# Kernel tuning notes

Measured on AMD Instinct MI355X. Metric: run time of the kernel, lower is better.

The kernel has to match this reference:

```python
import jax, jax.numpy as jnp
import numpy as np

B, H, S = 32, 128, 8192

def setup_inputs() -> dict:
    key = jax.random.key(0)
    k1, k2, k3, k4, k5 = jax.random.split(key, 5)
    return {
        "static_hidden": jax.random.normal(k1, (B, H, S), dtype=jnp.float32),
        "dynamic_hidden": jax.random.normal(k2, (B, H, S), dtype=jnp.float32),
        "decoder_hidden": jax.random.normal(k3, (B, H), dtype=jnp.float32),
        "v": jax.random.normal(k4, (1, 1, H), dtype=jnp.float32) * 0.01,
        "W": jax.random.normal(k5, (1, H, 3 * H), dtype=jnp.float32) * 0.01,
    }

def reference(static_hidden, dynamic_hidden, decoder_hidden, v, W):
    b, h, s = static_hidden.shape
    # concat (static, dynamic, expanded decoder) along feature dim -> [b, 3h, s]
    hidden = jnp.concatenate(
        [static_hidden, dynamic_hidden,
         jnp.broadcast_to(decoder_hidden[:, :, None], (b, h, s))], axis=1)
    # W[0]: [h, 3h]; tanh(W @ hidden) -> [b, h, s]
    e = jnp.tanh(jnp.einsum('hk,bks->bhs', W[0], hidden))
    # v[0,0]: [h]; scores -> [b, 1, s]
    scores = jnp.einsum('h,bhs->bs', v[0, 0], e)[:, None, :]
    return jax.nn.softmax(scores, axis=2)
```

## Files before the change

kernel.cpp:

```cpp
#include <hip/hip_runtime.h>
#include <math.h>

#define BB 32
#define HH 128
#define SS 8192

typedef __attribute__((ext_vector_type(8))) short bf8;
typedef __attribute__((ext_vector_type(4))) float f4;

static __device__ __forceinline__ unsigned short f2bf(float x) {
  union { float f; unsigned int u; } c; c.f = x;
  unsigned int r = c.u + 0x7FFFu + ((c.u >> 16) & 1u);
  return (unsigned short)(r >> 16);
}

__global__ __launch_bounds__(256) void prep_kernel(
    const float* __restrict__ W, const float* __restrict__ dec,
    unsigned short* __restrict__ Abf, float* __restrict__ bias) {
  const int b = blockIdx.x;
  const int tid = threadIdx.x;
  if (tid < HH) {
    const float* wr = W + (size_t)tid * 384 + 256;
    const float* db = dec + (size_t)b * HH;
    float acc = 0.f;
    #pragma unroll 8
    for (int j = 0; j < HH; ++j) acc += wr[j] * db[j];
    bias[b * HH + tid] = acc;
  }
  if (b == 0) {
    for (int idx = tid; idx < HH * 256; idx += 256) {
      int h = idx >> 8, k = idx & 255;
      Abf[idx] = f2bf(W[h * 384 + k]);
    }
  }
}

__global__ __launch_bounds__(256, 4) void attn_main(
    const float* __restrict__ sta, const float* __restrict__ dyn,
    const unsigned short* __restrict__ Abf, const float* __restrict__ bias,
    const float* __restrict__ v, float* __restrict__ scores) {
  const int tid  = threadIdx.x;
  const int l    = tid & 63;
  const int gw   = (blockIdx.x << 2) + (tid >> 6);
  const int b    = gw >> 8;
  const int tile = gw & 255;
  const int quad = l >> 4;
  const int n16  = l & 15;
  const int s0   = tile << 5;

  const size_t base = ((size_t)b << 20) + (size_t)(quad << 3) * SS + s0 + (n16 << 1);
  const float* p0 = sta + base;
  const float* p1 = dyn + base;

  f4 acc[8][2];
  #pragma unroll
  for (int mt = 0; mt < 8; ++mt) {
    acc[mt][0] = (f4){0.f, 0.f, 0.f, 0.f};
    acc[mt][1] = (f4){0.f, 0.f, 0.f, 0.f};
  }

  float2 bcur[8], bnxt[8];

  auto loadB = [&](int step, float2 (&dst)[8]) {
    const float* tp = (step < 4 ? p0 : p1) + ((size_t)((step & 3) << 5)) * SS;
    #pragma unroll
    for (int j = 0; j < 8; ++j)
      dst[j] = *(const float2*)(tp + (size_t)j * SS);
  };

  loadB(0, bcur);
  #pragma unroll
  for (int step = 0; step < 8; ++step) {
    if (step < 7) loadB(step + 1, bnxt);
    bf8 bfr0, bfr1;
    #pragma unroll
    for (int j = 0; j < 8; ++j) {
      bfr0[j] = (short)f2bf(bcur[j].x);
      bfr1[j] = (short)f2bf(bcur[j].y);
    }
    const unsigned short* abase = Abf + ((size_t)n16 << 8) + (step << 5) + (quad << 3);
    #pragma unroll
    for (int mt = 0; mt < 8; ++mt) {
      bf8 af = *(const bf8*)(abase + (mt << 12));
      acc[mt][0] = __builtin_amdgcn_mfma_f32_16x16x32_bf16(af, bfr0, acc[mt][0], 0, 0, 0);
      acc[mt][1] = __builtin_amdgcn_mfma_f32_16x16x32_bf16(af, bfr1, acc[mt][1], 0, 0, 0);
    }
    if (step < 7) {
      #pragma unroll
      for (int j = 0; j < 8; ++j) bcur[j] = bnxt[j];
    }
  }

  float part[2] = {0.f, 0.f};
  #pragma unroll
  for (int mt = 0; mt < 8; ++mt) {
    #pragma unroll
    for (int r = 0; r < 4; ++r) {
      const int h = mt * 16 + quad * 4 + r;
      const float bv = bias[(b << 7) + h];
      const float vv = v[h];
      part[0] += vv * tanhf(acc[mt][0][r] + bv);
      part[1] += vv * tanhf(acc[mt][1][r] + bv);
    }
  }
  part[0] += __shfl_xor(part[0], 16, 64);
  part[0] += __shfl_xor(part[0], 32, 64);
  part[1] += __shfl_xor(part[1], 16, 64);
  part[1] += __shfl_xor(part[1], 32, 64);
  if (quad == 0) {
    float2 o = make_float2(part[0], part[1]);
    *(float2*)(scores + ((size_t)b << 13) + s0 + (n16 << 1)) = o;
  }
}

__global__ __launch_bounds__(1024) void softmax_kernel(float* __restrict__ out) {
  const int b = blockIdx.x;
  const int tid = threadIdx.x;
  float* row = out + ((size_t)b << 13);
  float4 x0 = ((const float4*)row)[tid];
  float4 x1 = ((const float4*)row)[tid + 1024];
  float lmax = fmaxf(fmaxf(fmaxf(x0.x, x0.y), fmaxf(x0.z, x0.w)),
                     fmaxf(fmaxf(x1.x, x1.y), fmaxf(x1.z, x1.w)));
  __shared__ float red[17];
  #pragma unroll
  for (int o = 32; o >= 1; o >>= 1) lmax = fmaxf(lmax, __shfl_xor(lmax, o, 64));
  if ((tid & 63) == 0) red[tid >> 6] = lmax;
  __syncthreads();
  if (tid < 64) {
    float m = (tid < 16) ? red[tid] : -3.0e38f;
    #pragma unroll
    for (int o = 8; o >= 1; o >>= 1) m = fmaxf(m, __shfl_xor(m, o, 64));
    if (tid == 0) red[16] = m;
  }
  __syncthreads();
  const float gmax = red[16];
  float e[8];
  e[0] = expf(x0.x - gmax); e[1] = expf(x0.y - gmax);
  e[2] = expf(x0.z - gmax); e[3] = expf(x0.w - gmax);
  e[4] = expf(x1.x - gmax); e[5] = expf(x1.y - gmax);
  e[6] = expf(x1.z - gmax); e[7] = expf(x1.w - gmax);
  float ls = e[0] + e[1] + e[2] + e[3] + e[4] + e[5] + e[6] + e[7];
  #pragma unroll
  for (int o = 32; o >= 1; o >>= 1) ls += __shfl_xor(ls, o, 64);
  __syncthreads();
  if ((tid & 63) == 0) red[tid >> 6] = ls;
  __syncthreads();
  if (tid < 64) {
    float m = (tid < 16) ? red[tid] : 0.f;
    #pragma unroll
    for (int o = 8; o >= 1; o >>= 1) m += __shfl_xor(m, o, 64);
    if (tid == 0) red[16] = m;
  }
  __syncthreads();
  const float inv = 1.0f / red[16];
  float4 o0 = make_float4(e[0] * inv, e[1] * inv, e[2] * inv, e[3] * inv);
  float4 o1 = make_float4(e[4] * inv, e[5] * inv, e[6] * inv, e[7] * inv);
  ((float4*)row)[tid] = o0;
  ((float4*)row)[tid + 1024] = o1;
}

extern "C" void kernel_launch(void* const* d_in, const int* in_sizes, int n_in,
                              void* d_out, int out_size, void* d_ws, size_t ws_size,
                              hipStream_t stream) {
  const float* sta = (const float*)d_in[0];
  const float* dyn = (const float*)d_in[1];
  const float* dec = (const float*)d_in[2];
  const float* v   = (const float*)d_in[3];
  const float* W   = (const float*)d_in[4];

  unsigned short* Abf = (unsigned short*)d_ws;
  float* bias = (float*)((char*)d_ws + 128 * 256 * 2);
  float* scores = (float*)d_out;

  prep_kernel<<<BB, 256, 0, stream>>>(W, dec, Abf, bias);
  attn_main<<<BB * (SS / 32) / 4, 256, 0, stream>>>(sta, dyn, Abf, bias, v, scores);
  softmax_kernel<<<BB, 1024, 0, stream>>>(scores);
}
```

Baseline: 378.8 us.

## Stage bf16 weight matrix in swizzled LDS and widen blocks to 512 threads

Each 512-thread block now copies the full 128x256 bf16 weight matrix into shared memory with an XOR swizzle. The MFMA A-fragments are then read from LDS instead of global/L2. Block size doubles so each copy is amortized over eight waves. The B-operand conversion moves to after the MFMAs so it can overlap the next prefetch. The cost is 64KB of LDS per block, which may limit occupancy, plus a sync and copy at the start of every block.

Result: faster. 361.3 us (-4.6%).

```diff
diff --git a/kernel.cpp b/kernel.cpp
--- a/kernel.cpp
+++ b/kernel.cpp
@@ -7,6 +7,7 @@
 
 typedef __attribute__((ext_vector_type(8))) short bf8;
 typedef __attribute__((ext_vector_type(4))) float f4;
+typedef __attribute__((ext_vector_type(2))) float f2v;
 
 static __device__ __forceinline__ unsigned short f2bf(float x) {
   union { float f; unsigned int u; } c; c.f = x;
@@ -35,18 +36,29 @@
   }
 }
 
-__global__ __launch_bounds__(256, 4) void attn_main(
+__global__ __launch_bounds__(512, 4) void attn_main(
     const float* __restrict__ sta, const float* __restrict__ dyn,
     const unsigned short* __restrict__ Abf, const float* __restrict__ bias,
     const float* __restrict__ v, float* __restrict__ scores) {
+  __shared__ unsigned short LA[128 * 256];
+
   const int tid  = threadIdx.x;
   const int l    = tid & 63;
-  const int gw   = (blockIdx.x << 2) + (tid >> 6);
+  const int quad = l >> 4;
+  const int n16  = l & 15;
+  const int gw   = (blockIdx.x << 3) + (tid >> 6);
   const int b    = gw >> 8;
   const int tile = gw & 255;
-  const int quad = l >> 4;
-  const int n16  = l & 15;
   const int s0   = tile << 5;
+
+  #pragma unroll
+  for (int j = 0; j < 8; ++j) {
+    int gc = (j << 9) + tid;
+    int m = gc >> 5, ck = gc & 31;
+    bf8 val = *(const bf8*)(Abf + ((size_t)gc << 3));
+    *(bf8*)&LA[m * 256 + ((ck ^ (m & 7)) << 3)] = val;
+  }
+  __syncthreads();
 
   const size_t base = ((size_t)b << 20) + (size_t)(quad << 3) * SS + s0 + (n16 << 1);
   const float* p0 = sta + base;
@@ -59,36 +71,37 @@
     acc[mt][1] = (f4){0.f, 0.f, 0.f, 0.f};
   }
 
-  float2 bcur[8], bnxt[8];
+  f2v tmp[8];
+  bf8 cur0, cur1;
 
-  auto loadB = [&](int step, float2 (&dst)[8]) {
+  auto issueB = [&](int step) {
     const float* tp = (step < 4 ? p0 : p1) + ((size_t)((step & 3) << 5)) * SS;
     #pragma unroll
     for (int j = 0; j < 8; ++j)
-      dst[j] = *(const float2*)(tp + (size_t)j * SS);
+      tmp[j] = *(const f2v*)(tp + (size_t)j * SS);
+  };
+  auto conv = [&]() {
+    #pragma unroll
+    for (int j = 0; j < 8; ++j) {
+      cur0[j] = (short)f2bf(tmp[j].x);
+      cur1[j] = (short)f2bf(tmp[j].y);
+    }
   };
 
-  loadB(0, bcur);
+  const int swz = n16 & 7;
+  issueB(0);
+  conv();
   #pragma unroll
   for (int step = 0; step < 8; ++step) {
-    if (step < 7) loadB(step + 1, bnxt);
-    bf8 bfr0, bfr1;
-    #pragma unroll
-    for (int j = 0; j < 8; ++j) {
-      bfr0[j] = (short)f2bf(bcur[j].x);
-      bfr1[j] = (short)f2bf(bcur[j].y);
-    }
-    const unsigned short* abase = Abf + ((size_t)n16 << 8) + (step << 5) + (quad << 3);
+    if (step < 7) issueB(step + 1);
+    const int koff = (((step << 2) + quad) ^ swz) << 3;
     #pragma unroll
     for (int mt = 0; mt < 8; ++mt) {
-      bf8 af = *(const bf8*)(abase + (mt << 12));
-      acc[mt][0] = __builtin_amdgcn_mfma_f32_16x16x32_bf16(af, bfr0, acc[mt][0], 0, 0, 0);
-      acc[mt][1] = __builtin_amdgcn_mfma_f32_16x16x32_bf16(af, bfr1, acc[mt][1], 0, 0, 0);
+      bf8 af = *(const bf8*)&LA[(((mt << 4) + n16) << 8) + koff];
+      acc[mt][0] = __builtin_amdgcn_mfma_f32_16x16x32_bf16(af, cur0, acc[mt][0], 0, 0, 0);
+      acc[mt][1] = __builtin_amdgcn_mfma_f32_16x16x32_bf16(af, cur1, acc[mt][1], 0, 0, 0);
     }
-    if (step < 7) {
-      #pragma unroll
-      for (int j = 0; j < 8; ++j) bcur[j] = bnxt[j];
-    }
+    if (step < 7) conv();
   }
 
   float part[2] = {0.f, 0.f};
@@ -173,6 +186,6 @@
   float* scores = (float*)d_out;
 
   prep_kernel<<<BB, 256, 0, stream>>>(W, dec, Abf, bias);
-  attn_main<<<BB * (SS / 32) / 4, 256, 0, stream>>>(sta, dyn, Abf, bias, v, scores);
+  attn_main<<<BB * (SS / 32) / 8, 512, 0, stream>>>(sta, dyn, Abf, bias, v, scores);
   softmax_kernel<<<BB, 1024, 0, stream>>>(scores);
 }
```
